# Kernel tuning notes

Hardware: AMD Instinct MI355X
Metric: run time of the kernel (lower is better)

The kernel has to match this reference:

```python
import jax, jax.numpy as jnp
import numpy as np

B, S, N, D = 8, 2048, 512, 1024
MAX_W = 32  # fixed max span width (inclusive widths 0..MAX_W-1)
MASK_FILL = -1000.0


def setup_inputs() -> dict:
    key = jax.random.key(0)
    k1, k2, k3, k4 = jax.random.split(key, 4)
    sequence_tensor = jax.random.normal(k1, (B, S, D), dtype=jnp.float32)
    starts = jax.random.randint(k2, (B, N), 0, S - MAX_W)
    widths = jax.random.randint(k3, (B, N), 0, MAX_W)  # inclusive width = widths
    span_indices = jnp.stack([starts, starts + widths], axis=-1)  # (B, N, 2)
    att_w = jax.random.normal(k4, (D, 1), dtype=jnp.float32) * 0.02
    att_b = jnp.zeros((1,), dtype=jnp.float32)
    return {"sequence_tensor": sequence_tensor, "span_indices": span_indices,
            "att_w": att_w, "att_b": att_b}


def reference(sequence_tensor, span_indices, att_w, att_b):
    dtype = sequence_tensor.dtype
    starts = span_indices[..., 0]               # (B, N)
    ends = span_indices[..., 1]                 # (B, N), inclusive
    widths = ends - starts                      # (B, N)

    rng = jnp.arange(MAX_W)                     # (W,)
    raw_idx = ends[..., None] - rng             # (B, N, W), walks backward from end
    span_mask = (rng <= widths[..., None]) & (raw_idx >= 0)  # (B, N, W)
    idx = jnp.maximum(raw_idx, 0)               # relu on indices

    # global attention logits: (B, S, 1)
    logits = sequence_tensor @ att_w + att_b

    b, n = idx.shape[0], idx.shape[1]
    flat = idx.reshape(b, n * MAX_W)            # (B, N*W)
    # gather embeddings and logits over the time axis
    span_emb = jnp.take_along_axis(sequence_tensor, flat[..., None], axis=1)
    span_emb = span_emb.reshape(b, n, MAX_W, -1)              # (B, N, W, D)
    span_logits = jnp.take_along_axis(logits[..., 0], flat, axis=1)
    span_logits = span_logits.reshape(b, n, MAX_W)            # (B, N, W)

    # memory-efficient masked softmax: fill masked logits with -1000
    masked_logits = jnp.where(span_mask, span_logits, jnp.asarray(MASK_FILL, dtype))
    attn = jax.nn.softmax(masked_logits, axis=-1)             # (B, N, W)

    # weighted-sum pooling over span positions
    return jnp.einsum('bnw,bnwd->bnd', attn, span_emb)
```

## Files before the change

### kernel.cpp

```cpp
#include <hip/hip_runtime.h>
#include <hip/hip_bf16.h>

#define B 8
#define S 2048
#define N 512
#define D 1024
#define MAX_W 32
#define MASK_FILL -1000.0f

__global__ __launch_bounds__(256) void logits_kernel(
    const float* __restrict__ seq,
    const float* __restrict__ att_w,
    const float* __restrict__ att_b,
    float* __restrict__ logits)
{
    const int row  = blockIdx.x * 4 + (threadIdx.x >> 6);
    const int lane = threadIdx.x & 63;

    const float4* rp = (const float4*)(seq + (size_t)row * D);
    const float4* wp = (const float4*)att_w;

    float acc = 0.0f;
#pragma unroll
    for (int k = 0; k < 4; ++k) {
        const float4 a = rp[lane + 64 * k];
        const float4 w = wp[lane + 64 * k];
        acc += a.x * w.x + a.y * w.y + a.z * w.z + a.w * w.w;
    }

#pragma unroll
    for (int off = 32; off > 0; off >>= 1)
        acc += __shfl_down(acc, off);

    if (lane == 0)
        logits[row] = acc + att_b[0];
}

__global__ __launch_bounds__(256) void pool_kernel(
    const float* __restrict__ seq,
    const int*   __restrict__ spans,
    const float* __restrict__ logits,
    float* __restrict__ out)
{
    const int span = blockIdx.x;
    const int b    = span / N;

    const int start = spans[2 * span + 0];
    const int end   = spans[2 * span + 1];
    const int width = end - start;

    __shared__ float s_attn[MAX_W];
    __shared__ int   s_idx[MAX_W];

    const int tid = threadIdx.x;

    if (tid < MAX_W) {
        const int w   = tid;
        const int raw = end - w;
        const bool valid = (w <= width) && (raw >= 0);
        const int idx = raw > 0 ? raw : 0;
        const float l = valid ? logits[b * S + idx] : MASK_FILL;

        float m = l;
#pragma unroll
        for (int off = 16; off > 0; off >>= 1)
            m = fmaxf(m, __shfl_down(m, off, 32));
        m = __shfl(m, 0, 32);

        const float p = __expf(l - m);

        float sum = p;
#pragma unroll
        for (int off = 16; off > 0; off >>= 1)
            sum += __shfl_down(sum, off, 32);
        sum = __shfl(sum, 0, 32);

        s_attn[w] = p / sum;
        s_idx[w]  = idx;
    }
    __syncthreads();

    const size_t seq_base = (size_t)b * S;
    float4 acc = make_float4(0.f, 0.f, 0.f, 0.f);

    const int cnt = width + 1;
    for (int w = 0; w < cnt; ++w) {
        const float a = s_attn[w];
        const float4 v =
            ((const float4*)(seq + (seq_base + (size_t)s_idx[w]) * D))[tid];
        acc.x += a * v.x;
        acc.y += a * v.y;
        acc.z += a * v.z;
        acc.w += a * v.w;
    }

    ((float4*)(out + (size_t)span * D))[tid] = acc;
}

extern "C" void kernel_launch(void* const* d_in, const int* in_sizes, int n_in,
                              void* d_out, int out_size, void* d_ws, size_t ws_size,
                              hipStream_t stream)
{
    const float* seq    = (const float*)d_in[0];
    const int*   spans  = (const int*)  d_in[1];
    const float* att_w  = (const float*)d_in[2];
    const float* att_b  = (const float*)d_in[3];

    float* out    = (float*)d_out;
    float* logits = (float*)d_ws;

    logits_kernel<<<(B * S) / 4, 256, 0, stream>>>(seq, att_w, att_b, logits);
    pool_kernel<<<B * N, 256, 0, stream>>>(seq, spans, logits, out);
}
```

Before: 138.2 us.

## Unroll span pooling by four, interleave batches across blocks, nontemporal output stores

The pooling loop now rounds the span width up to a multiple of four and issues four independent row loads per iteration, so more memory requests are in flight. Padded positions read rows whose softmax weight is tiny (masked, exp of about -1000), so they contribute roughly zero but still cost extra bandwidth. Block indices are remapped so consecutive blocks cover different batches. The output is written with nontemporal stores to avoid polluting the cache.

New measurement: 123.3 us. 1.12x faster.

```diff
diff --git a/kernel.cpp b/kernel.cpp
--- a/kernel.cpp
+++ b/kernel.cpp
@@ -7,6 +7,8 @@
 #define D 1024
 #define MAX_W 32
 #define MASK_FILL -1000.0f
+
+typedef float vfloat4 __attribute__((ext_vector_type(4)));
 
 __global__ __launch_bounds__(256) void logits_kernel(
     const float* __restrict__ seq,
@@ -42,8 +44,9 @@
     const float* __restrict__ logits,
     float* __restrict__ out)
 {
-    const int span = blockIdx.x;
-    const int b    = span / N;
+    const int b    = blockIdx.x & 7;
+    const int n    = blockIdx.x >> 3;
+    const int span = b * N + n;
 
     const int start = spans[2 * span + 0];
     const int end   = spans[2 * span + 1];
@@ -80,21 +83,37 @@
     }
     __syncthreads();
 
-    const size_t seq_base = (size_t)b * S;
+    const float* sb = seq + (size_t)b * S * D;
     float4 acc = make_float4(0.f, 0.f, 0.f, 0.f);
 
-    const int cnt = width + 1;
-    for (int w = 0; w < cnt; ++w) {
-        const float a = s_attn[w];
-        const float4 v =
-            ((const float4*)(seq + (seq_base + (size_t)s_idx[w]) * D))[tid];
-        acc.x += a * v.x;
-        acc.y += a * v.y;
-        acc.z += a * v.z;
-        acc.w += a * v.w;
+    const int cnt  = width + 1;
+    const int cnt4 = (cnt + 3) & ~3;
+
+    for (int w = 0; w < cnt4; w += 4) {
+        const float a0 = s_attn[w + 0];
+        const float a1 = s_attn[w + 1];
+        const float a2 = s_attn[w + 2];
+        const float a3 = s_attn[w + 3];
+        const int   i0 = s_idx[w + 0];
+        const int   i1 = s_idx[w + 1];
+        const int   i2 = s_idx[w + 2];
+        const int   i3 = s_idx[w + 3];
+
+        const float4 v0 = ((const float4*)(sb + (size_t)i0 * D))[tid];
+        const float4 v1 = ((const float4*)(sb + (size_t)i1 * D))[tid];
+        const float4 v2 = ((const float4*)(sb + (size_t)i2 * D))[tid];
+        const float4 v3 = ((const float4*)(sb + (size_t)i3 * D))[tid];
+
+        acc.x += a0 * v0.x + a1 * v1.x + a2 * v2.x + a3 * v3.x;
+        acc.y += a0 * v0.y + a1 * v1.y + a2 * v2.y + a3 * v3.y;
+        acc.z += a0 * v0.z + a1 * v1.z + a2 * v2.z + a3 * v3.z;
+        acc.w += a0 * v0.w + a1 * v1.w + a2 * v2.w + a3 * v3.w;
     }
 
-    ((float4*)(out + (size_t)span * D))[tid] = acc;
+    vfloat4 vacc;
+    vacc.x = acc.x; vacc.y = acc.y; vacc.z = acc.z; vacc.w = acc.w;
+    vfloat4* op = ((vfloat4*)(out + (size_t)span * D)) + tid;
+    __builtin_nontemporal_store(vacc, op);
 }
 
 extern "C" void kernel_launch(void* const* d_in, const int* in_sizes, int n_in,
```
